# Optimization experiments

Measured on AMD Instinct MI355X. Metric: run time of the kernel, lower is better.

## Reference

```python
import jax, jax.numpy as jnp
import numpy as np

K_NN = 9  # kernel_size: neighbors per node (includes self, dist 0)


def knn_edges(feat):
    """feat: (B, C, N). Replicates DenseDilatedKnnGraph (dilation=1):
    L2-normalize over channels, dense pairwise sq-distance, top-k nearest."""
    nrm = jnp.sqrt(jnp.sum(feat * feat, axis=1, keepdims=True))
    xn = feat / jnp.maximum(nrm, 1e-12)            # F.normalize(dim=1)
    xt = jnp.swapaxes(xn, 1, 2)                    # (B, N, C)
    sq = jnp.sum(xt * xt, axis=-1)                 # (B, N)
    dist = sq[:, :, None] + sq[:, None, :] - 2.0 * jnp.einsum('bnc,bmc->bnm', xt, xt)
    _, nn_idx = jax.lax.top_k(-dist, K_NN)         # (B, N, k)
    center = jnp.broadcast_to(jnp.arange(nn_idx.shape[1], dtype=nn_idx.dtype)[None, :, None], nn_idx.shape)
    return nn_idx, center                          # (x_j sources, x_i targets)


def reference(x, W0, W1, bias):
    B, C, H, W = x.shape
    N = H * W
    NB = B * N
    feat = x.reshape(B, C, N)
    # KNN graph is built on detached features in the torch source
    x_j, x_i = knn_edges(jax.lax.stop_gradient(feat))
    E = B * N * K_NN
    # faithful to source: torch.linspace(0, B, steps=E, dtype=int64) batch offsets
    count = jnp.linspace(0.0, float(B), E).astype(jnp.int32)
    src = x_j.reshape(-1).astype(jnp.int32) + count * N
    dst = x_i.reshape(-1).astype(jnp.int32) + count * N
    valid = (src < NB) & (dst < NB)                # drop the out-of-range tail edge
    # flat_nodes: (B, C, H, W) -> (B*H*W, C), node id = b*HW + pixel
    nodes = jnp.swapaxes(feat, 1, 2).reshape(NB, C)
    # ChebConv K=2, sym norm, lambda_max=2: Tx0 = x, Tx1 = -(D^-1/2 A D^-1/2) x
    w = valid.astype(nodes.dtype)
    deg = jax.ops.segment_sum(w, src, num_segments=NB)
    dinv = jnp.where(deg > 0, jax.lax.rsqrt(jnp.maximum(deg, 1.0)), 0.0)
    norm = -(dinv[src] * w * dinv[dst])            # scaled-Laplacian edge weights
    msg = norm[:, None] * nodes[src]               # (E, C) gather + weight
    Tx1 = jax.ops.segment_sum(msg, dst, num_segments=NB)
    return nodes @ W0 + Tx1 @ W1 + bias


def setup_inputs() -> dict:
    key = jax.random.key(0)
    k1, k2, k3, k4 = jax.random.split(key, 4)
    B, C, H, W = 8, 48, 64, 64
    Cout = 48
    s = 1.0 / np.sqrt(C)
    return {
        'x': jax.random.normal(k1, (B, C, H, W), dtype=jnp.float32),
        'W0': jax.random.normal(k2, (C, Cout), dtype=jnp.float32) * s,
        'W1': jax.random.normal(k3, (C, Cout), dtype=jnp.float32) * s,
        'bias': jax.random.normal(k4, (Cout,), dtype=jnp.float32) * 0.01,
    }
```

## Files before the change

kernel.cpp:

```cpp
#include <hip/hip_runtime.h>

#define BATCH 8
#define CH    48
#define NPTS  4096
#define NBN   (BATCH*NPTS)
#define KNN   9
#define NCAND 12

typedef unsigned short u16;
typedef unsigned int   u32;
typedef unsigned long long u64;
typedef __bf16 bf16x8 __attribute__((ext_vector_type(8)));
typedef float  f32x4  __attribute__((ext_vector_type(4)));

__device__ __forceinline__ float bf2f(u16 v) { return __uint_as_float(((u32)v) << 16); }
__device__ __forceinline__ u16 f2bf(float f) {
  u32 u = __float_as_uint(f);
  u = (u + 0x7fffu + ((u >> 16) & 1u)) >> 16;
  return (u16)u;
}

#define MED3U(d, a, b, c) \
  asm("v_med3_u32 %0, %1, %2, %3" : "=v"(d) : "v"(a), "v"(b), "v"(c))
#define INS12(p0,p1,p2,p3,p4,p5,p6,p7,p8,p9,p10,p11,x) do { \
  MED3U(p11,p10,p11,x); MED3U(p10,p9,p10,x); MED3U(p9,p8,p9,x);  \
  MED3U(p8, p7, p8, x); MED3U(p7, p6,p7, x); MED3U(p6,p5,p6,x);  \
  MED3U(p5, p4, p5, x); MED3U(p4, p3,p4, x); MED3U(p3,p2,p3,x);  \
  MED3U(p2, p1, p2, x); MED3U(p1, p0,p1, x); p0 = min(p0, x);    \
} while (0)

__device__ __forceinline__ void stage_q(const u16* g, u16* l) {
  __builtin_amdgcn_global_load_lds(
      (const __attribute__((address_space(1))) void*)g,
      (__attribute__((address_space(3))) void*)l, 16, 0, 0);
}

__global__ __launch_bounds__(256)
void k_prep(const float* __restrict__ x, float* __restrict__ xraw,
            float* __restrict__ xn, float* __restrict__ csq,
            u16* __restrict__ Abuf, u16* __restrict__ Bbuf,
            int* __restrict__ deg) {
  int node = blockIdx.x * 256 + threadIdx.x;
  deg[node] = 0;
  int b = node >> 12, n = node & (NPTS - 1);
  const float* xb = x + (size_t)b * CH * NPTS;
  float f[CH];
#pragma unroll
  for (int c = 0; c < CH; ++c) f[c] = xb[(size_t)c * NPTS + n];
  float a0 = 0, a1 = 0, a2 = 0, a3 = 0;
#pragma unroll
  for (int k = 0; k < CH; k += 4) {
    a0 += f[k] * f[k]; a1 += f[k+1] * f[k+1];
    a2 += f[k+2] * f[k+2]; a3 += f[k+3] * f[k+3];
  }
  float nrm = fmaxf(sqrtf((a0 + a1) + (a2 + a3)), 1e-12f);
  float xv[CH];
#pragma unroll
  for (int c = 0; c < CH; ++c) xv[c] = f[c] / nrm;
  a0 = a1 = a2 = a3 = 0;
#pragma unroll
  for (int k = 0; k < CH; k += 4) {
    a0 += xv[k] * xv[k]; a1 += xv[k+1] * xv[k+1];
    a2 += xv[k+2] * xv[k+2]; a3 += xv[k+3] * xv[k+3];
  }
  float csqv = (a0 + a1) + (a2 + a3);
  csq[node] = csqv;
  float4* ro = (float4*)(xraw + (size_t)node * CH);
  float4* no = (float4*)(xn   + (size_t)node * CH);
#pragma unroll
  for (int i = 0; i < CH / 4; ++i) {
    ro[i] = make_float4(f[4*i], f[4*i+1], f[4*i+2], f[4*i+3]);
    no[i] = make_float4(xv[4*i], xv[4*i+1], xv[4*i+2], xv[4*i+3]);
  }
  u16 ah[64], al[64];
#pragma unroll
  for (int k = 0; k < CH; ++k) {
    float av = -2.0f * xv[k];
    u16 h = f2bf(av); ah[k] = h; al[k] = f2bf(av - bf2f(h));
  }
  { u16 h = f2bf(csqv); ah[48] = h; al[48] = f2bf(csqv - bf2f(h)); }
#pragma unroll
  for (int k = 49; k < 64; ++k) { ah[k] = 0; al[k] = 0; }
  u16* Bh = Bbuf + (size_t)node * 128;
#pragma unroll
  for (int k = 0; k < CH; ++k) {
    float bv = xv[k];
    u16 h = f2bf(bv); Bh[k] = h; Bh[64 + k] = f2bf(bv - bf2f(h));
  }
  Bh[48] = 0x3F80; Bh[64 + 48] = 0;
#pragma unroll
  for (int k = 49; k < 64; ++k) { Bh[k] = 0; Bh[64 + k] = 0; }
  u16* Ag = Abuf + (size_t)(node >> 4) * 2048 + (size_t)(node & 15) * 8;
#pragma unroll
  for (int v = 0; v < 4; ++v) {
    const u16* src = (v < 2) ? ah : al;
    int koff = (v & 1) * 32;
#pragma unroll
    for (int q = 0; q < 4; ++q) {
      uint4 pk;
      const u16* s = src + koff + q * 8;
      pk.x = (u32)s[0] | ((u32)s[1] << 16);
      pk.y = (u32)s[2] | ((u32)s[3] << 16);
      pk.z = (u32)s[4] | ((u32)s[5] << 16);
      pk.w = (u32)s[6] | ((u32)s[7] << 16);
      *(uint4*)(Ag + v * 512 + q * 128) = pk;
    }
  }
}

__global__ __launch_bounds__(256, 6)
void k_knn_m(const u16* __restrict__ Abuf, const u16* __restrict__ Bbuf,
             u32* __restrict__ candu) {
  __shared__ __align__(16) u16 As[2][2][2048];
  int tid = threadIdx.x;
  int lane = tid & 63;
  int wv = tid >> 6;
  int quad = lane >> 4, m16 = lane & 15;
  int panel = blockIdx.x * 4 + wv;
  int row = panel * 16 + m16;
  int b4096 = row & ~(NPTS - 1);
  int quarter = blockIdx.y;
  int ct0 = quarter * 64;

  const __bf16* Bb = (const __bf16*)Bbuf + (size_t)row * 128;
  bf16x8 bh0 = *(const bf16x8*)(Bb + quad * 8);
  bf16x8 bh1 = *(const bf16x8*)(Bb + 32 + quad * 8);
  bf16x8 bl0 = *(const bf16x8*)(Bb + 64 + quad * 8);
  bf16x8 bl1 = *(const bf16x8*)(Bb + 96 + quad * 8);

  const u16* gs = Abuf + ((size_t)(b4096 >> 4) + ct0) * 2048
                  + wv * 512 + lane * 8;

  u32 s0=~0u,s1=~0u,s2=~0u,s3=~0u,s4=~0u,s5=~0u,
      s6=~0u,s7=~0u,s8=~0u,s9=~0u,s10=~0u,s11=~0u;

  const f32x4 C25 = {2.5f, 2.5f, 2.5f, 2.5f};

#define LDA(P, S, A0,A1,A2,A3) do {                                         \
    const u16* _p = &As[P][S][lane * 8];                                    \
    A0 = *(const bf16x8*)(_p);                                              \
    A1 = *(const bf16x8*)(_p + 512);                                        \
    A2 = *(const bf16x8*)(_p + 1024);                                       \
    A3 = *(const bf16x8*)(_p + 1536);                                       \
  } while (0)
#define MFMA6(ACC, A0,A1,A2,A3) do {                                        \
    ACC = __builtin_amdgcn_mfma_f32_16x16x32_bf16(A0, bh0, C25, 0, 0, 0);   \
    ACC = __builtin_amdgcn_mfma_f32_16x16x32_bf16(A1, bh1, ACC, 0, 0, 0);   \
    ACC = __builtin_amdgcn_mfma_f32_16x16x32_bf16(A0, bl0, ACC, 0, 0, 0);   \
    ACC = __builtin_amdgcn_mfma_f32_16x16x32_bf16(A1, bl1, ACC, 0, 0, 0);   \
    ACC = __builtin_amdgcn_mfma_f32_16x16x32_bf16(A2, bh0, ACC, 0, 0, 0);   \
    ACC = __builtin_amdgcn_mfma_f32_16x16x32_bf16(A3, bh1, ACC, 0, 0, 0);   \
  } while (0)
#define FILTER(ACC, CT) do {                                                \
    u32 _colb = ((u32)(CT) << 4) | ((u32)quad << 2);                        \
    _Pragma("unroll")                                                       \
    for (int _r = 0; _r < 4; ++_r) {                                        \
      u32 _u = __float_as_uint((ACC)[_r]);                                  \
      u32 _x = (_u & 0xFFFFF000u) | (_colb | (u32)_r);                      \
      INS12(s0,s1,s2,s3,s4,s5,s6,s7,s8,s9,s10,s11, _x);                     \
    }                                                                       \
  } while (0)

  f32x4 accA, accB;
  bf16x8 a0, a1, a2, a3;

  stage_q(gs,        &As[0][0][wv * 512]);
  stage_q(gs + 2048, &As[0][1][wv * 512]);
  __syncthreads();

  LDA(0, 0, a0, a1, a2, a3);
  stage_q(gs + (size_t)2 * 2048, &As[1][0][wv * 512]);
  stage_q(gs + (size_t)3 * 2048, &As[1][1][wv * 512]);
  MFMA6(accA, a0, a1, a2, a3);
  LDA(0, 1, a0, a1, a2, a3);
  MFMA6(accB, a0, a1, a2, a3);
  FILTER(accA, ct0 + 0);
  __syncthreads();

  for (int p = 1; p < 31; ++p) {
    int par = p & 1;
    LDA(par, 0, a0, a1, a2, a3);
    stage_q(gs + (size_t)(2 * p + 2) * 2048, &As[par ^ 1][0][wv * 512]);
    stage_q(gs + (size_t)(2 * p + 3) * 2048, &As[par ^ 1][1][wv * 512]);
    MFMA6(accA, a0, a1, a2, a3);
    FILTER(accB, ct0 + 2 * p - 1);
    LDA(par, 1, a0, a1, a2, a3);
    MFMA6(accB, a0, a1, a2, a3);
    FILTER(accA, ct0 + 2 * p);
    __syncthreads();
  }
  LDA(1, 0, a0, a1, a2, a3);
  MFMA6(accA, a0, a1, a2, a3);
  FILTER(accB, ct0 + 61);
  LDA(1, 1, a0, a1, a2, a3);
  MFMA6(accB, a0, a1, a2, a3);
  FILTER(accA, ct0 + 62);
  FILTER(accB, ct0 + 63);
#undef LDA
#undef MFMA6
#undef FILTER

  u32* o = candu + (((size_t)row * 4 + quarter) * 4 + quad) * NCAND;
  o[0]=s0; o[1]=s1; o[2]=s2; o[3]=s3; o[4]=s4; o[5]=s5;
  o[6]=s6; o[7]=s7; o[8]=s8; o[9]=s9; o[10]=s10; o[11]=s11;
}

__global__ __launch_bounds__(256, 4)
void k_reduce(const u32* __restrict__ candu, u32* __restrict__ cand12) {
  __shared__ __align__(16) u32 ls[64 * 4 * NCAND];
  int tid = threadIdx.x;
  int lr = tid >> 2, q = tid & 3;
  int row = blockIdx.x * 64 + lr;
  const uint4* src = (const uint4*)(candu + (size_t)row * 192 + q * 48);
  u32 t0=~0u,t1=~0u,t2=~0u,t3=~0u,t4=~0u,t5=~0u,
      t6=~0u,t7=~0u,t8=~0u,t9=~0u,t10=~0u,t11=~0u;
  for (int s = 0; s < 12; ++s) {
    uint4 v = src[s];
    INS12(t0,t1,t2,t3,t4,t5,t6,t7,t8,t9,t10,t11, v.x);
    INS12(t0,t1,t2,t3,t4,t5,t6,t7,t8,t9,t10,t11, v.y);
    INS12(t0,t1,t2,t3,t4,t5,t6,t7,t8,t9,t10,t11, v.z);
    INS12(t0,t1,t2,t3,t4,t5,t6,t7,t8,t9,t10,t11, v.w);
  }
  u32* lw = ls + (size_t)(lr * 4 + q) * NCAND;
  lw[0]=t0; lw[1]=t1; lw[2]=t2; lw[3]=t3; lw[4]=t4; lw[5]=t5;
  lw[6]=t6; lw[7]=t7; lw[8]=t8; lw[9]=t9; lw[10]=t10; lw[11]=t11;
  __syncthreads();
  if (q == 0) {
    u32 g0=~0u,g1=~0u,g2=~0u,g3=~0u,g4=~0u,g5=~0u,
        g6=~0u,g7=~0u,g8=~0u,g9=~0u,g10=~0u,g11=~0u;
    const uint4* lsrc = (const uint4*)(ls + (size_t)lr * 48);
    for (int s = 0; s < 12; ++s) {
      uint4 v = lsrc[s];
      INS12(g0,g1,g2,g3,g4,g5,g6,g7,g8,g9,g10,g11, v.x);
      INS12(g0,g1,g2,g3,g4,g5,g6,g7,g8,g9,g10,g11, v.y);
      INS12(g0,g1,g2,g3,g4,g5,g6,g7,g8,g9,g10,g11, v.z);
      INS12(g0,g1,g2,g3,g4,g5,g6,g7,g8,g9,g10,g11, v.w);
    }
    u32* o = cand12 + (size_t)row * NCAND;
    o[0]=(g0&0xFFFu); o[1]=(g1&0xFFFu); o[2]=(g2&0xFFFu);
    o[3]=(g3&0xFFFu); o[4]=(g4&0xFFFu); o[5]=(g5&0xFFFu);
    o[6]=(g6&0xFFFu); o[7]=(g7&0xFFFu); o[8]=(g8&0xFFFu);
    o[9]=(g9&0xFFFu); o[10]=(g10&0xFFFu); o[11]=(g11&0xFFFu);
  }
}

#define RR 16
__global__ __launch_bounds__(256, 4)
void k_rescore(const float* __restrict__ xn, const float* __restrict__ csq,
               const u32* __restrict__ cand12,
               u16* __restrict__ nn, int* __restrict__ deg) {
  __shared__ float dS[RR * NCAND];
  __shared__ int   iS[RR * NCAND];
  int tid = threadIdx.x;
  int lr = tid >> 4, q = tid & 15;
  int bi = blockIdx.x;
  int row = (bi & 7) * NPTS + (bi >> 3) * RR + lr;
  int b4096 = row & ~(NPTS - 1);
  const float* xnb = xn + (size_t)b4096 * CH;
  if (q < NCAND) {
    float rf[CH];
    const float4* p = (const float4*)(xn + (size_t)row * CH);
#pragma unroll
    for (int i = 0; i < CH / 4; ++i) {
      float4 v = p[i];
      rf[4*i] = v.x; rf[4*i+1] = v.y; rf[4*i+2] = v.z; rf[4*i+3] = v.w;
    }
    float sqn = csq[row];
    int c = (int)(cand12[(size_t)row * NCAND + q] & (NPTS - 1));
    const float4* cp = (const float4*)(xnb + (size_t)c * CH);
    float a0 = 0, a1 = 0, a2 = 0, a3 = 0;
#pragma unroll
    for (int i = 0; i < CH / 4; ++i) {
      float4 v = cp[i];
      a0 += rf[4*i]   * v.x; a1 += rf[4*i+1] * v.y;
      a2 += rf[4*i+2] * v.z; a3 += rf[4*i+3] * v.w;
    }
    float dist = (sqn + csq[b4096 + c]) - 2.0f * ((a0 + a1) + (a2 + a3));
    dS[lr * NCAND + q] = dist;
    iS[lr * NCAND + q] = c;
  }
  __syncthreads();
  if (q == 0) {
    float gd[KNN]; int gi[KNN];
#pragma unroll
    for (int j = 0; j < KNN; ++j) { gd[j] = 3.4e38f; gi[j] = 0x7fffffff; }
    for (int s = 0; s < NCAND; ++s) {
      float dc = dS[lr * NCAND + s]; int ic = iS[lr * NCAND + s];
      if (dc < gd[KNN - 1] || (dc == gd[KNN - 1] && ic < gi[KNN - 1])) {
        gd[KNN - 1] = dc; gi[KNN - 1] = ic;
#pragma unroll
        for (int k2 = KNN - 1; k2 > 0; --k2) {
          bool sw = (gd[k2] < gd[k2 - 1]) ||
                    (gd[k2] == gd[k2 - 1] && gi[k2] < gi[k2 - 1]);
          if (sw) {
            float td = gd[k2]; gd[k2] = gd[k2 - 1]; gd[k2 - 1] = td;
            int ti = gi[k2]; gi[k2] = gi[k2 - 1]; gi[k2 - 1] = ti;
          }
        }
      }
    }
    u16* o = nn + (size_t)row * KNN;
    int jmax = (row == NBN - 1) ? (KNN - 1) : KNN;
#pragma unroll
    for (int j = 0; j < KNN; ++j) o[j] = (u16)(gi[j] & (NPTS - 1));
    for (int j = 0; j < jmax; ++j)
      atomicAdd(&deg[b4096 + (gi[j] & (NPTS - 1))], 1);
  }
}

#define ONB 64
#define LPAD 52
__global__ __launch_bounds__(256)
void k_out_f(const float* __restrict__ xraw, const u16* __restrict__ nn,
             const int* __restrict__ deg,
             const float* __restrict__ W0, const float* __restrict__ W1,
             const float* __restrict__ bias, float* __restrict__ out) {
  __shared__ float w0[CH * CH], w1[CH * CH], bs[CH];
  __shared__ __align__(16) float fS[ONB * LPAD];
  __shared__ __align__(16) float txS[ONB * LPAD];
  __shared__ float dinvS[ONB];
  int tid = threadIdx.x;
  int bi = blockIdx.x;
  int n0 = (bi & 7) * NPTS + (bi >> 3) * ONB;
  int b12 = n0 & ~(NPTS - 1);
  for (int i = tid; i < CH * CH; i += 256) { w0[i] = W0[i]; w1[i] = W1[i]; }
  if (tid < CH) bs[tid] = bias[tid];
  for (int i = tid; i < ONB * 12; i += 256) {
    int ln = i / 12, f4 = i % 12;
    *(float4*)(fS + ln * LPAD + f4 * 4) =
        *(const float4*)(xraw + (size_t)(n0 + ln) * CH + f4 * 4);
  }
  if (tid < ONB) {
    int dg = deg[n0 + tid];
    dinvS[tid] = (dg > 0) ? (1.0f / sqrtf((float)dg)) : 0.0f;
  }
  __syncthreads();

  int ln = tid >> 2, p = tid & 3;
  int node = n0 + ln;
  float dn = dinvS[ln];
  const u16* nrow = nn + (size_t)node * KNN;
  bool full = (node != NBN - 1);
  float tx[12];
#pragma unroll
  for (int i = 0; i < 12; ++i) tx[i] = 0.f;
#pragma unroll
  for (int j = 0; j < KNN; ++j) {
    if (j < KNN - 1 || full) {
      int s = nrow[j] & (NPTS - 1);
      int dgs = deg[b12 + s];
      float ds = (dgs > 0) ? (1.0f / sqrtf((float)dgs)) : 0.0f;
      float w = -(ds * dn);
      const float4* pr = (const float4*)(xraw + (size_t)(b12 + s) * CH + p * 12);
#pragma unroll
      for (int q3 = 0; q3 < 3; ++q3) {
        float4 v = pr[q3];
        tx[q3*4]   += w * v.x; tx[q3*4+1] += w * v.y;
        tx[q3*4+2] += w * v.z; tx[q3*4+3] += w * v.w;
      }
    }
  }
#pragma unroll
  for (int q3 = 0; q3 < 3; ++q3)
    *(float4*)(txS + ln * LPAD + p * 12 + q3 * 4) =
        make_float4(tx[q3*4], tx[q3*4+1], tx[q3*4+2], tx[q3*4+3]);
  __syncthreads();

  float acc[12];
#pragma unroll
  for (int i = 0; i < 12; ++i) acc[i] = bs[p * 12 + i];
  const float* fr = fS + ln * LPAD;
  const float* tr = txS + ln * LPAD;
#pragma unroll
  for (int c = 0; c < CH; ++c) {
    float fc = fr[c];
    const float* wr = w0 + c * CH + p * 12;
#pragma unroll
    for (int i = 0; i < 12; ++i) acc[i] += fc * wr[i];
  }
#pragma unroll
  for (int c = 0; c < CH; ++c) {
    float tc = tr[c];
    const float* wr = w1 + c * CH + p * 12;
#pragma unroll
    for (int i = 0; i < 12; ++i) acc[i] += tc * wr[i];
  }
  float* op = out + (size_t)node * CH + p * 12;
#pragma unroll
  for (int q3 = 0; q3 < 3; ++q3)
    *(float4*)(op + q3 * 4) =
        make_float4(acc[q3*4], acc[q3*4+1], acc[q3*4+2], acc[q3*4+3]);
}

__global__ __launch_bounds__(256)
void k_zero(int* __restrict__ deg) { deg[blockIdx.x * 256 + threadIdx.x] = 0; }

__global__ __launch_bounds__(256)
void k_hist(const u16* __restrict__ nn, int* __restrict__ deg) {
  int node = blockIdx.x * 256 + threadIdx.x;
  int b12 = node & ~(NPTS - 1);
  int jmax = (node == NBN - 1) ? (KNN - 1) : KNN;
  for (int j = 0; j < jmax; ++j)
    atomicAdd(&deg[b12 + (nn[(size_t)node * KNN + j] & (NPTS - 1))], 1);
}

__global__ __launch_bounds__(256)
void k_dinv(const int* __restrict__ deg, float* __restrict__ dinv) {
  int i = blockIdx.x * 256 + threadIdx.x;
  int dg = deg[i];
  dinv[i] = (dg > 0) ? (1.0f / sqrtf((float)dg)) : 0.0f;
}

#define NQ    4
#define QCOLS (NPTS/NQ)
#define TCOLS 32
#define NTILES (QCOLS/TCOLS)
#define RPB   64

__global__ __launch_bounds__(256)
void k_knn_nb(const float* __restrict__ x, u16* __restrict__ nn) {
  __shared__ __align__(16) float tile[NQ * TCOLS * CH];
  __shared__ float nrmS[NQ * TCOLS];
  __shared__ float csq[NQ * TCOLS];
  int tid = threadIdx.x;
  int r0 = blockIdx.x * RPB;
  int b  = r0 >> 12;
  int q  = tid >> 6;
  int lr = tid & 63;
  int n  = (r0 + lr) & (NPTS - 1);
  const float* xb = x + (size_t)b * CH * NPTS;
  float rf[CH];
#pragma unroll
  for (int c = 0; c < CH; ++c) rf[c] = xb[(size_t)c * NPTS + n];
  float sqn;
  {
    float a0 = 0, a1 = 0, a2 = 0, a3 = 0;
#pragma unroll
    for (int k = 0; k < CH; k += 4) {
      a0 += rf[k] * rf[k]; a1 += rf[k+1] * rf[k+1];
      a2 += rf[k+2] * rf[k+2]; a3 += rf[k+3] * rf[k+3];
    }
    float nrm = fmaxf(sqrtf((a0 + a1) + (a2 + a3)), 1e-12f);
#pragma unroll
    for (int c = 0; c < CH; ++c) rf[c] = rf[c] / nrm;
    a0 = a1 = a2 = a3 = 0;
#pragma unroll
    for (int k = 0; k < CH; k += 4) {
      a0 += rf[k] * rf[k]; a1 += rf[k+1] * rf[k+1];
      a2 += rf[k+2] * rf[k+2]; a3 += rf[k+3] * rf[k+3];
    }
    sqn = (a0 + a1) + (a2 + a3);
  }
  float d[KNN]; int id[KNN];
#pragma unroll
  for (int j = 0; j < KNN; ++j) { d[j] = 3.4e38f; id[j] = 0x7fffffff; }
  for (int t = 0; t < NTILES; ++t) {
    __syncthreads();
#pragma unroll
    for (int qq = 0; qq < NQ; ++qq) {
      int colbase = qq * QCOLS + t * TCOLS;
      float* dst = tile + qq * TCOLS * CH;
#pragma unroll
      for (int it = 0; it < 6; ++it) {
        int i = it * 256 + tid;
        int c = i >> 5, p = i & 31;
        dst[p * CH + c] = xb[(size_t)c * NPTS + colbase + p];
      }
    }
    __syncthreads();
    if (tid < NQ * TCOLS) {
      const float* cp = tile + tid * CH;
      float a0 = 0, a1 = 0, a2 = 0, a3 = 0;
#pragma unroll
      for (int k = 0; k < CH; k += 4) {
        float4 v = *(const float4*)(cp + k);
        a0 += v.x * v.x; a1 += v.y * v.y; a2 += v.z * v.z; a3 += v.w * v.w;
      }
      nrmS[tid] = fmaxf(sqrtf((a0 + a1) + (a2 + a3)), 1e-12f);
    }
    __syncthreads();
    for (int i = tid; i < NQ * TCOLS * CH; i += 256)
      tile[i] = tile[i] / nrmS[i / CH];
    __syncthreads();
    if (tid < NQ * TCOLS) {
      const float* cp = tile + tid * CH;
      float a0 = 0, a1 = 0, a2 = 0, a3 = 0;
#pragma unroll
      for (int k = 0; k < CH; k += 4) {
        float4 v = *(const float4*)(cp + k);
        a0 += v.x * v.x; a1 += v.y * v.y; a2 += v.z * v.z; a3 += v.w * v.w;
      }
      csq[tid] = (a0 + a1) + (a2 + a3);
    }
    __syncthreads();
    int cbase = q * QCOLS + t * TCOLS;
    const float* tq = tile + q * TCOLS * CH;
    for (int cc = 0; cc < TCOLS; ++cc) {
      const float* cp = tq + cc * CH;
      float a0 = 0, a1 = 0, a2 = 0, a3 = 0;
#pragma unroll
      for (int k = 0; k < CH; k += 4) {
        float4 v = *(const float4*)(cp + k);
        a0 += rf[k] * v.x; a1 += rf[k+1] * v.y;
        a2 += rf[k+2] * v.z; a3 += rf[k+3] * v.w;
      }
      float dist = (sqn + csq[q * TCOLS + cc]) - 2.0f * ((a0 + a1) + (a2 + a3));
      if (dist < d[KNN - 1]) {
        d[KNN - 1] = dist; id[KNN - 1] = cbase + cc;
#pragma unroll
        for (int k2 = KNN - 1; k2 > 0; --k2) {
          if (d[k2] < d[k2 - 1]) {
            float td = d[k2]; d[k2] = d[k2 - 1]; d[k2 - 1] = td;
            int ti = id[k2]; id[k2] = id[k2 - 1]; id[k2 - 1] = ti;
          }
        }
      }
    }
  }
  __syncthreads();
  float* md = tile;
  int*   mi = (int*)(tile + 256 * KNN);
#pragma unroll
  for (int j = 0; j < KNN; ++j) { md[tid * KNN + j] = d[j]; mi[tid * KNN + j] = id[j]; }
  __syncthreads();
  if (tid < RPB) {
    float fd[KNN]; int fi[KNN];
#pragma unroll
    for (int j = 0; j < KNN; ++j) { fd[j] = 3.4e38f; fi[j] = 0x7fffffff; }
    for (int qq = 0; qq < NQ; ++qq) {
      int s = qq * RPB + tid;
      for (int j = 0; j < KNN; ++j) {
        float dc = md[s * KNN + j]; int ic = mi[s * KNN + j];
        if (dc < fd[KNN - 1]) {
          fd[KNN - 1] = dc; fi[KNN - 1] = ic;
#pragma unroll
          for (int k2 = KNN - 1; k2 > 0; --k2) {
            if (fd[k2] < fd[k2 - 1]) {
              float td = fd[k2]; fd[k2] = fd[k2 - 1]; fd[k2 - 1] = td;
              int ti = fi[k2]; fi[k2] = fi[k2 - 1]; fi[k2 - 1] = ti;
            }
          }
        }
      }
    }
    u16* o = nn + (size_t)(r0 + tid) * KNN;
#pragma unroll
    for (int j = 0; j < KNN; ++j) o[j] = (u16)(fi[j] & (NPTS - 1));
  }
}

__global__ __launch_bounds__(256)
void k_out_nb(const float* __restrict__ x, const u16* __restrict__ nn,
              const float* __restrict__ dinv,
              const float* __restrict__ W0, const float* __restrict__ W1,
              const float* __restrict__ bias, float* __restrict__ out) {
  __shared__ float w0[CH * CH], w1[CH * CH], bs[CH];
  for (int i = threadIdx.x; i < CH * CH; i += 256) { w0[i] = W0[i]; w1[i] = W1[i]; }
  if (threadIdx.x < CH) bs[threadIdx.x] = bias[threadIdx.x];
  __syncthreads();
  int node = blockIdx.x * 256 + threadIdx.x;
  int b = node >> 12, n = node & (NPTS - 1);
  const float* xb = x + (size_t)b * CH * NPTS;
  float f[CH], acc[CH], tx[CH];
#pragma unroll
  for (int c = 0; c < CH; ++c) f[c] = xb[(size_t)c * NPTS + n];
#pragma unroll
  for (int o = 0; o < CH; ++o) acc[o] = bs[o];
#pragma unroll
  for (int c = 0; c < CH; ++c) {
    float fc = f[c];
    const float* wr = w0 + c * CH;
#pragma unroll
    for (int o = 0; o < CH; ++o) acc[o] += fc * wr[o];
  }
#pragma unroll
  for (int c = 0; c < CH; ++c) tx[c] = 0.f;
  float dn = dinv[node];
  int jmax = (node == NBN - 1) ? (KNN - 1) : KNN;
  for (int j = 0; j < jmax; ++j) {
    int s = nn[(size_t)node * KNN + j] & (NPTS - 1);
    float w = -(dinv[(b << 12) + s] * dn);
#pragma unroll
    for (int c = 0; c < CH; ++c) tx[c] += w * xb[(size_t)c * NPTS + s];
  }
#pragma unroll
  for (int c = 0; c < CH; ++c) {
    float tc = tx[c];
    const float* wr = w1 + c * CH;
#pragma unroll
    for (int o = 0; o < CH; ++o) acc[o] += tc * wr[o];
  }
  float4* op = (float4*)(out + (size_t)node * CH);
#pragma unroll
  for (int i = 0; i < CH / 4; ++i)
    op[i] = make_float4(acc[4*i], acc[4*i+1], acc[4*i+2], acc[4*i+3]);
}

extern "C" void kernel_launch(void* const* d_in, const int* in_sizes, int n_in,
                              void* d_out, int out_size, void* d_ws, size_t ws_size,
                              hipStream_t stream) {
  const float* x    = (const float*)d_in[0];
  const float* W0   = (const float*)d_in[1];
  const float* W1   = (const float*)d_in[2];
  const float* bias = (const float*)d_in[3];
  float* out = (float*)d_out;
  char* w = (char*)d_ws;

  const size_t SZ_XN   = (size_t)NBN * CH * 4;
  const size_t SZ_XRAW = (size_t)NBN * CH * 4;
  const size_t SZ_CSQ  = (size_t)NBN * 4;
  const size_t SZ_NN   = (size_t)NBN * KNN * 2;
  const size_t SZ_DEG  = (size_t)NBN * 4;
  const size_t SZ_AB   = (size_t)NBN * 128 * 2;
  const size_t SZ_CU   = (size_t)NBN * 16 * NCAND * 4;
  const size_t SZ_C12  = (size_t)NBN * NCAND * 4;
  const size_t needF = SZ_XN + SZ_XRAW + SZ_CSQ + SZ_NN + SZ_DEG
                     + 2 * SZ_AB + SZ_CU + SZ_C12;

  if (ws_size >= needF) {
    size_t off = 0;
    float* xn   = (float*)(w + off); off += SZ_XN;
    float* xraw = (float*)(w + off); off += SZ_XRAW;
    float* csq  = (float*)(w + off); off += SZ_CSQ;
    u16*   nn   = (u16*)  (w + off); off += SZ_NN;
    int*   deg  = (int*)  (w + off); off += SZ_DEG;
    u16*   Abuf = (u16*)  (w + off); off += SZ_AB;
    u16*   Bbuf = (u16*)  (w + off); off += SZ_AB;
    u32*   candu= (u32*)  (w + off); off += SZ_CU;
    u32*   cand12=(u32*)  (w + off);
    k_prep    <<<NBN / 256, 256, 0, stream>>>(x, xraw, xn, csq, Abuf, Bbuf, deg);
    k_knn_m   <<<dim3(NBN / 64, 4), 256, 0, stream>>>(Abuf, Bbuf, candu);
    k_reduce  <<<NBN / 64, 256, 0, stream>>>(candu, cand12);
    k_rescore <<<NBN / RR, 256, 0, stream>>>(xn, csq, cand12, nn, deg);
    k_out_f   <<<NBN / ONB, 256, 0, stream>>>(xraw, nn, deg, W0, W1, bias, out);
  } else {
    u16*   nn   = (u16*)w;
    int*   deg  = (int*)(w + SZ_NN);
    float* dinv = (float*)(w + SZ_NN + SZ_DEG);
    k_knn_nb <<<NBN / RPB, 256, 0, stream>>>(x, nn);
    k_zero   <<<NBN / 256, 256, 0, stream>>>(deg);
    k_hist   <<<NBN / 256, 256, 0, stream>>>(nn, deg);
    k_dinv   <<<NBN / 256, 256, 0, stream>>>(deg, dinv);
    k_out_nb <<<NBN / 256, 256, 0, stream>>>(x, nn, dinv, W0, W1, bias, out);
  }
}
```

Before: 208.2 us.

## Split KNN column range into halves and streamline prep packing

The KNN MFMA kernel now covers 128 column tiles per block in two halves instead of 64 tiles in four quarters. This halves the candidate buffer and the reduce input, and gives longer pipelined loops per block, at the cost of fewer blocks in the grid. The prep kernel replaces its per-element division with a reciprocal multiply. It packs the bf16 hi/lo splits straight into uint4 stores instead of building large u16 arrays, and it launches 64-thread blocks to ease register pressure.

```diff
diff --git a/kernel.cpp b/kernel.cpp
--- a/kernel.cpp
+++ b/kernel.cpp
@@ -35,12 +35,12 @@
       (__attribute__((address_space(3))) void*)l, 16, 0, 0);
 }
 
-__global__ __launch_bounds__(256)
+__global__ __launch_bounds__(64)
 void k_prep(const float* __restrict__ x, float* __restrict__ xraw,
             float* __restrict__ xn, float* __restrict__ csq,
             u16* __restrict__ Abuf, u16* __restrict__ Bbuf,
             int* __restrict__ deg) {
-  int node = blockIdx.x * 256 + threadIdx.x;
+  int node = blockIdx.x * 64 + threadIdx.x;
   deg[node] = 0;
   int b = node >> 12, n = node & (NPTS - 1);
   const float* xb = x + (size_t)b * CH * NPTS;
@@ -54,14 +54,12 @@
     a2 += f[k+2] * f[k+2]; a3 += f[k+3] * f[k+3];
   }
   float nrm = fmaxf(sqrtf((a0 + a1) + (a2 + a3)), 1e-12f);
-  float xv[CH];
-#pragma unroll
-  for (int c = 0; c < CH; ++c) xv[c] = f[c] / nrm;
+  float rn = 1.0f / nrm;
   a0 = a1 = a2 = a3 = 0;
 #pragma unroll
   for (int k = 0; k < CH; k += 4) {
-    a0 += xv[k] * xv[k]; a1 += xv[k+1] * xv[k+1];
-    a2 += xv[k+2] * xv[k+2]; a3 += xv[k+3] * xv[k+3];
+    float v0 = f[k]*rn, v1 = f[k+1]*rn, v2 = f[k+2]*rn, v3 = f[k+3]*rn;
+    a0 += v0*v0; a1 += v1*v1; a2 += v2*v2; a3 += v3*v3;
   }
   float csqv = (a0 + a1) + (a2 + a3);
   csq[node] = csqv;
@@ -70,41 +68,45 @@
 #pragma unroll
   for (int i = 0; i < CH / 4; ++i) {
     ro[i] = make_float4(f[4*i], f[4*i+1], f[4*i+2], f[4*i+3]);
-    no[i] = make_float4(xv[4*i], xv[4*i+1], xv[4*i+2], xv[4*i+3]);
-  }
-  u16 ah[64], al[64];
-#pragma unroll
-  for (int k = 0; k < CH; ++k) {
-    float av = -2.0f * xv[k];
-    u16 h = f2bf(av); ah[k] = h; al[k] = f2bf(av - bf2f(h));
-  }
-  { u16 h = f2bf(csqv); ah[48] = h; al[48] = f2bf(csqv - bf2f(h)); }
-#pragma unroll
-  for (int k = 49; k < 64; ++k) { ah[k] = 0; al[k] = 0; }
-  u16* Bh = Bbuf + (size_t)node * 128;
-#pragma unroll
-  for (int k = 0; k < CH; ++k) {
-    float bv = xv[k];
-    u16 h = f2bf(bv); Bh[k] = h; Bh[64 + k] = f2bf(bv - bf2f(h));
-  }
-  Bh[48] = 0x3F80; Bh[64 + 48] = 0;
-#pragma unroll
-  for (int k = 49; k < 64; ++k) { Bh[k] = 0; Bh[64 + k] = 0; }
+    no[i] = make_float4(f[4*i]*rn, f[4*i+1]*rn, f[4*i+2]*rn, f[4*i+3]*rn);
+  }
+  uint4* Bo = (uint4*)(Bbuf + (size_t)node * 128);
   u16* Ag = Abuf + (size_t)(node >> 4) * 2048 + (size_t)(node & 15) * 8;
 #pragma unroll
-  for (int v = 0; v < 4; ++v) {
-    const u16* src = (v < 2) ? ah : al;
-    int koff = (v & 1) * 32;
-#pragma unroll
-    for (int q = 0; q < 4; ++q) {
-      uint4 pk;
-      const u16* s = src + koff + q * 8;
-      pk.x = (u32)s[0] | ((u32)s[1] << 16);
-      pk.y = (u32)s[2] | ((u32)s[3] << 16);
-      pk.z = (u32)s[4] | ((u32)s[5] << 16);
-      pk.w = (u32)s[6] | ((u32)s[7] << 16);
-      *(uint4*)(Ag + v * 512 + q * 128) = pk;
-    }
+  for (int g = 0; g < 6; ++g) {
+    u32 bhw[4], blw[4], ahw[4], alw[4];
+#pragma unroll
+    for (int j = 0; j < 4; ++j) {
+      int k = g * 8 + j * 2;
+      float v0 = f[k] * rn, v1 = f[k+1] * rn;
+      u16 h0 = f2bf(v0), h1 = f2bf(v1);
+      u16 l0 = f2bf(v0 - bf2f(h0)), l1 = f2bf(v1 - bf2f(h1));
+      bhw[j] = (u32)h0 | ((u32)h1 << 16);
+      blw[j] = (u32)l0 | ((u32)l1 << 16);
+      float w0 = -2.0f * v0, w1 = -2.0f * v1;
+      u16 g0 = f2bf(w0), g1 = f2bf(w1);
+      u16 m0 = f2bf(w0 - bf2f(g0)), m1 = f2bf(w1 - bf2f(g1));
+      ahw[j] = (u32)g0 | ((u32)g1 << 16);
+      alw[j] = (u32)m0 | ((u32)m1 << 16);
+    }
+    Bo[g]     = make_uint4(bhw[0], bhw[1], bhw[2], bhw[3]);
+    Bo[8 + g] = make_uint4(blw[0], blw[1], blw[2], blw[3]);
+    int v = g >> 2, q = g & 3;
+    *(uint4*)(Ag + v * 512 + q * 128)        = make_uint4(ahw[0], ahw[1], ahw[2], ahw[3]);
+    *(uint4*)(Ag + 1024 + v * 512 + q * 128) = make_uint4(alw[0], alw[1], alw[2], alw[3]);
+  }
+  {
+    u16 h = f2bf(csqv); u16 l = f2bf(csqv - bf2f(h));
+    Bo[6]  = make_uint4(0x3F80u, 0, 0, 0);
+    Bo[14] = make_uint4(0, 0, 0, 0);
+    *(uint4*)(Ag + 512 + 2 * 128)        = make_uint4((u32)h, 0, 0, 0);
+    *(uint4*)(Ag + 1024 + 512 + 2 * 128) = make_uint4((u32)l, 0, 0, 0);
+  }
+  {
+    uint4 z = make_uint4(0, 0, 0, 0);
+    Bo[7] = z; Bo[15] = z;
+    *(uint4*)(Ag + 512 + 3 * 128)        = z;
+    *(uint4*)(Ag + 1024 + 512 + 3 * 128) = z;
   }
 }
 
@@ -119,8 +121,8 @@
   int panel = blockIdx.x * 4 + wv;
   int row = panel * 16 + m16;
   int b4096 = row & ~(NPTS - 1);
-  int quarter = blockIdx.y;
-  int ct0 = quarter * 64;
+  int half = blockIdx.y;
+  int ct0 = half * 128;
 
   const __bf16* Bb = (const __bf16*)Bbuf + (size_t)row * 128;
   bf16x8 bh0 = *(const bf16x8*)(Bb + quad * 8);
@@ -177,7 +179,7 @@
   FILTER(accA, ct0 + 0);
   __syncthreads();
 
-  for (int p = 1; p < 31; ++p) {
+  for (int p = 1; p < 63; ++p) {
     int par = p & 1;
     LDA(par, 0, a0, a1, a2, a3);
     stage_q(gs + (size_t)(2 * p + 2) * 2048, &As[par ^ 1][0][wv * 512]);
@@ -191,16 +193,16 @@
   }
   LDA(1, 0, a0, a1, a2, a3);
   MFMA6(accA, a0, a1, a2, a3);
-  FILTER(accB, ct0 + 61);
+  FILTER(accB, ct0 + 125);
   LDA(1, 1, a0, a1, a2, a3);
   MFMA6(accB, a0, a1, a2, a3);
-  FILTER(accA, ct0 + 62);
-  FILTER(accB, ct0 + 63);
+  FILTER(accA, ct0 + 126);
+  FILTER(accB, ct0 + 127);
 #undef LDA
 #undef MFMA6
 #undef FILTER
 
-  u32* o = candu + (((size_t)row * 4 + quarter) * 4 + quad) * NCAND;
+  u32* o = candu + (((size_t)row * 2 + half) * 4 + quad) * NCAND;
   o[0]=s0; o[1]=s1; o[2]=s2; o[3]=s3; o[4]=s4; o[5]=s5;
   o[6]=s6; o[7]=s7; o[8]=s8; o[9]=s9; o[10]=s10; o[11]=s11;
 }
@@ -211,10 +213,10 @@
   int tid = threadIdx.x;
   int lr = tid >> 2, q = tid & 3;
   int row = blockIdx.x * 64 + lr;
-  const uint4* src = (const uint4*)(candu + (size_t)row * 192 + q * 48);
+  const uint4* src = (const uint4*)(candu + (size_t)row * 96 + q * 24);
   u32 t0=~0u,t1=~0u,t2=~0u,t3=~0u,t4=~0u,t5=~0u,
       t6=~0u,t7=~0u,t8=~0u,t9=~0u,t10=~0u,t11=~0u;
-  for (int s = 0; s < 12; ++s) {
+  for (int s = 0; s < 6; ++s) {
     uint4 v = src[s];
     INS12(t0,t1,t2,t3,t4,t5,t6,t7,t8,t9,t10,t11, v.x);
     INS12(t0,t1,t2,t3,t4,t5,t6,t7,t8,t9,t10,t11, v.y);
@@ -612,7 +614,7 @@
   const size_t SZ_NN   = (size_t)NBN * KNN * 2;
   const size_t SZ_DEG  = (size_t)NBN * 4;
   const size_t SZ_AB   = (size_t)NBN * 128 * 2;
-  const size_t SZ_CU   = (size_t)NBN * 16 * NCAND * 4;
+  const size_t SZ_CU   = (size_t)NBN * 8 * NCAND * 4;
   const size_t SZ_C12  = (size_t)NBN * NCAND * 4;
   const size_t needF = SZ_XN + SZ_XRAW + SZ_CSQ + SZ_NN + SZ_DEG
                      + 2 * SZ_AB + SZ_CU + SZ_C12;
@@ -628,8 +630,8 @@
     u16*   Bbuf = (u16*)  (w + off); off += SZ_AB;
     u32*   candu= (u32*)  (w + off); off += SZ_CU;
     u32*   cand12=(u32*)  (w + off);
-    k_prep    <<<NBN / 256, 256, 0, stream>>>(x, xraw, xn, csq, Abuf, Bbuf, deg);
-    k_knn_m   <<<dim3(NBN / 64, 4), 256, 0, stream>>>(Abuf, Bbuf, candu);
+    k_prep    <<<NBN / 64, 64, 0, stream>>>(x, xraw, xn, csq, Abuf, Bbuf, deg);
+    k_knn_m   <<<dim3(NBN / 64, 2), 256, 0, stream>>>(Abuf, Bbuf, candu);
     k_reduce  <<<NBN / 64, 256, 0, stream>>>(candu, cand12);
     k_rescore <<<NBN / RR, 256, 0, stream>>>(xn, csq, cand12, nn, deg);
     k_out_f   <<<NBN / ONB, 256, 0, stream>>>(xraw, nn, deg, W0, W1, bias, out);
```

After: 206.7 us. About the same (-0.7%).
